# Kernel optimization log

Hardware: AMD Instinct MI355X
Metric: run time of the kernel (lower is better)

## Reference

```python
import jax, jax.numpy as jnp
import numpy as np

N, CT, C, L, H, W, HEAD, GROUPS = 4, 512, 512, 256, 64, 64, 16, 16


def setup_inputs() -> dict:
    key = jax.random.key(0)
    ks = jax.random.split(key, 8)
    d_in_g = C // GROUPS
    return {
        "feature": jax.random.normal(ks[0], (N, C, H, W), dtype=jnp.float32),
        "token": jax.random.normal(ks[1], (N, CT, L), dtype=jnp.float32),
        # conv1x1_1d value/key projections: weight [C_out, C_in]
        "Wv": jax.random.normal(ks[2], (C, CT), dtype=jnp.float32) * (1.0 / np.sqrt(CT)),
        "bv": jnp.zeros((C,), dtype=jnp.float32),
        "Wk": jax.random.normal(ks[3], (C, CT), dtype=jnp.float32) * (1.0 / np.sqrt(CT)),
        "bk": jnp.zeros((C,), dtype=jnp.float32),
        # grouped conv1x1_2d query projection: weight [groups, C_out/g, C_in/g]
        "Wq": jax.random.normal(ks[4], (GROUPS, d_in_g, d_in_g), dtype=jnp.float32) * (1.0 / np.sqrt(d_in_g)),
        "bq": jnp.zeros((C,), dtype=jnp.float32),
    }


def reference(feature, token, Wv, bv, Wk, bk, Wq, bq):
    h = HEAD
    d = C // h              # per-head dim
    S = H * W               # query positions
    # value / key: 1x1 conv1d == matmul over channel dim
    proj_v = (jnp.einsum('oc,ncl->nol', Wv, token) + bv[None, :, None]).reshape(N, h, d, L)
    proj_k = (jnp.einsum('oc,ncl->nol', Wk, token) + bk[None, :, None]).reshape(N, h, d, L)
    # query: grouped 1x1 conv2d (padding=0; see notes) == per-group matmul
    f_g = feature.reshape(N, GROUPS, C // GROUPS, S)
    q = jnp.einsum('goi,ngis->ngos', Wq, f_g).reshape(N, C, S) + bq[None, :, None]
    proj_q = q.reshape(N, h, d, S).transpose(0, 1, 3, 2)  # [N, h, S, d]
    scale = 1.0 / np.sqrt(C / h)
    scores = jnp.einsum('nhsd,nhdl->nhsl', proj_q, proj_k) * scale  # [N,h,S,L]
    proj_coef = jax.nn.softmax(scores, axis=3)
    proj = jnp.einsum('nhdl,nhsl->nhds', proj_v, proj_coef)  # [N,h,d,S]
    return feature + proj.reshape(N, C, H, W)
```

## Files before the change

### kernel.cpp

```cpp
#include <hip/hip_runtime.h>

typedef float f32x4 __attribute__((ext_vector_type(4)));
typedef short bf16x8 __attribute__((ext_vector_type(8)));
typedef __bf16 bf2 __attribute__((ext_vector_type(2)));
typedef unsigned short u16;
typedef unsigned int u32;

#define CT_ 512
#define C_ 512
#define L_ 256
#define S_ 4096
#define D_ 32

static __device__ __forceinline__ u16 f2bf(float x) {
    union { __bf16 h; u16 u; } v; v.h = (__bf16)x; return v.u;
}
static __device__ __forceinline__ u32 packbf(float a, float b) {
    union { bf2 h; u32 u; } v;
    v.h[0] = (__bf16)a; v.h[1] = (__bf16)b;
    return v.u;
}

__global__ __launch_bounds__(256) void prep_all(const float* __restrict__ Wv,
                                                const float* __restrict__ Wk,
                                                const float* __restrict__ token,
                                                u16* __restrict__ wbf,
                                                u16* __restrict__ tokT) {
    __shared__ float tile[32][33];
    int bx = blockIdx.x;
    int t = threadIdx.x;
    if (bx < 256) {
        int idx = (bx * 256 + t) * 8;
        const float* src = (idx < 262144) ? (Wv + idx) : (Wk + (idx - 262144));
        float4 a = *(const float4*)src;
        float4 b = *(const float4*)(src + 4);
        uint4 o;
        o.x = packbf(a.x, a.y);
        o.y = packbf(a.z, a.w);
        o.z = packbf(b.x, b.y);
        o.w = packbf(b.z, b.w);
        *(uint4*)(wbf + idx) = o;
    } else {
        int b2 = bx - 256;
        int ct_t = b2 & 15, l_t = (b2 >> 4) & 7, n = b2 >> 7;
        int r = t >> 3, c4 = (t & 7) * 4;
        const float* src = token + ((size_t)n * CT_ + ct_t * 32 + r) * L_ + l_t * 32 + c4;
        float4 v = *(const float4*)src;
        tile[r][c4] = v.x; tile[r][c4 + 1] = v.y; tile[r][c4 + 2] = v.z; tile[r][c4 + 3] = v.w;
        __syncthreads();
        uint2 o;
        o.x = packbf(tile[c4][r],     tile[c4 + 1][r]);
        o.y = packbf(tile[c4 + 2][r], tile[c4 + 3][r]);
        *(uint2*)(tokT + ((size_t)n * L_ + l_t * 32 + r) * CT_ + ct_t * 32 + c4) = o;
    }
}

__global__ __launch_bounds__(64) void kv_gemm(const u16* __restrict__ Wv_bf,
                                              const u16* __restrict__ Wk_bf,
                                              const u16* __restrict__ tokT,
                                              const float* __restrict__ bv,
                                              const float* __restrict__ bk,
                                              u16* __restrict__ V_hs,
                                              u16* __restrict__ KT_hs) {
    int bx = blockIdx.x;
    int xcd = bx & 7, slot = bx >> 3;
    int l_t = slot & 7, hb = (slot >> 3) & 1, kv = (slot >> 4) & 1, n = slot >> 5;
    int c_t = (hb << 3) | xcd;
    const u16* W = kv ? Wk_bf : Wv_bf;
    const float* bias = kv ? bk : bv;
    int c0 = c_t * 32, l0 = l_t * 32;
    int lane = threadIdx.x;
    int lr = lane & 15, g = lane >> 4;

    const f32x4 fz = {0.f, 0.f, 0.f, 0.f};
    f32x4 acc[2][2] = {{fz, fz}, {fz, fz}};

    const u16* Abase = W + (size_t)(c0 + lr) * CT_ + g * 8;
    const u16* Bbase = tokT + ((size_t)n * L_ + l0 + lr) * CT_ + g * 8;

#pragma unroll
    for (int k = 0; k < 16; ++k) {
        bf16x8 a0 = *(const bf16x8*)(Abase + k * 32);
        bf16x8 a1 = *(const bf16x8*)(Abase + (size_t)16 * CT_ + k * 32);
        bf16x8 b0 = *(const bf16x8*)(Bbase + k * 32);
        bf16x8 b1 = *(const bf16x8*)(Bbase + (size_t)16 * CT_ + k * 32);
        acc[0][0] = __builtin_amdgcn_mfma_f32_16x16x32_bf16(a0, b0, acc[0][0], 0, 0, 0);
        acc[0][1] = __builtin_amdgcn_mfma_f32_16x16x32_bf16(a0, b1, acc[0][1], 0, 0, 0);
        acc[1][0] = __builtin_amdgcn_mfma_f32_16x16x32_bf16(a1, b0, acc[1][0], 0, 0, 0);
        acc[1][1] = __builtin_amdgcn_mfma_f32_16x16x32_bf16(a1, b1, acc[1][1], 0, 0, 0);
    }

    float bb[2][4];
#pragma unroll
    for (int ci = 0; ci < 2; ++ci)
#pragma unroll
        for (int r = 0; r < 4; ++r) bb[ci][r] = bias[c0 + ci * 16 + g * 4 + r];

    if (kv == 0) {
#pragma unroll
        for (int ci = 0; ci < 2; ++ci)
#pragma unroll
            for (int jt = 0; jt < 2; ++jt) {
                int o = jt * 16 + lr;
                int c = o >> 2, q = o & 3;
                int ip = ((c >> 2) & 1) | ((c & 3) << 1);
                int dst_l = l0 + ip * 4 + q;
#pragma unroll
                for (int r = 0; r < 4; ++r) {
                    int d = ci * 16 + g * 4 + r;
                    V_hs[(((size_t)n * 16 + c_t) * D_ + d) * L_ + dst_l] =
                        f2bf(acc[ci][jt][r] + bb[ci][r]);
                }
            }
    } else {
#pragma unroll
        for (int jt = 0; jt < 2; ++jt) {
            int l = l0 + jt * 16 + lr;
#pragma unroll
            for (int ci = 0; ci < 2; ++ci) {
                uint2 o;
                o.x = packbf(acc[ci][jt][0] + bb[ci][0], acc[ci][jt][1] + bb[ci][1]);
                o.y = packbf(acc[ci][jt][2] + bb[ci][2], acc[ci][jt][3] + bb[ci][3]);
                *(uint2*)(KT_hs + (((size_t)n * 16 + c_t) * L_ + l) * D_
                          + g * 8 + ci * 4) = o;
            }
        }
    }
}

__global__ __launch_bounds__(256, 4) void attn(const float* __restrict__ feature,
                                               const float* __restrict__ Wq,
                                               const float* __restrict__ bq,
                                               const u16* __restrict__ V_hs,
                                               const u16* __restrict__ KT_hs,
                                               float* __restrict__ out) {
    __shared__ u16 KT_lds[256][40];
    __shared__ u16 V_lds[32][296];

    int bx = blockIdx.x;
    int xcd = bx & 7, slot = bx >> 3;
    int sb = slot & 31, hb = (slot >> 5) & 1, n = slot >> 6;
    int h = (hb << 3) | xcd;
    int s_base = sb * 128;
    int t = threadIdx.x;
    int w = t >> 6, lane = t & 63, lr = lane & 15, g = lane >> 4;
    const f32x4 fz = {0.f, 0.f, 0.f, 0.f};

    {
        const u16* kbase = KT_hs + ((size_t)n * 16 + h) * (L_ * D_);
#pragma unroll
        for (int i = 0; i < 4; ++i) {
            uint4 v = *(const uint4*)(kbase + ((size_t)i * 256 + t) * 8);
            *(uint4*)&KT_lds[i * 64 + (t >> 2)][(t & 3) * 8] = v;
        }
    }
    {
        const u16* vbase = V_hs + ((size_t)n * 16 + h) * (D_ * L_);
#pragma unroll
        for (int i = 0; i < 4; ++i) {
            uint4 v = *(const uint4*)(vbase + ((size_t)i * 256 + t) * 8);
            *(uint4*)&V_lds[i * 8 + (t >> 5)][(t & 31) * 8] = v;
        }
    }

    const float scale = 0.17677669529663687f * 1.4426950408889634f;
    union { u32 d[4]; bf16x8 v; } wqf[2];
#pragma unroll
    for (int dt = 0; dt < 2; ++dt) {
        const float* wsrc = Wq + ((size_t)h * D_ + dt * 16 + lr) * D_ + g * 8;
        float4 w0 = *(const float4*)wsrc;
        float4 w1 = *(const float4*)(wsrc + 4);
        wqf[dt].d[0] = packbf(w0.x * scale, w0.y * scale);
        wqf[dt].d[1] = packbf(w0.z * scale, w0.w * scale);
        wqf[dt].d[2] = packbf(w1.x * scale, w1.y * scale);
        wqf[dt].d[3] = packbf(w1.z * scale, w1.w * scale);
    }
    f32x4 bqc[2];
#pragma unroll
    for (int dt = 0; dt < 2; ++dt)
#pragma unroll
        for (int r = 0; r < 4; ++r)
            bqc[dt][r] = bq[h * D_ + dt * 16 + g * 4 + r] * scale;

    const float* fb = feature + ((size_t)n * C_ + h * D_) * S_ + s_base + w * 16 + lr;
    float f0[8], f1[8];
#pragma unroll
    for (int j = 0; j < 8; ++j) f0[j] = fb[(size_t)(g * 8 + j) * S_];
#pragma unroll
    for (int j = 0; j < 8; ++j) f1[j] = fb[(size_t)(g * 8 + j) * S_ + 64];

    __syncthreads();

#pragma unroll
    for (int tile = 0; tile < 2; ++tile) {
        int s0 = s_base + tile * 64;

        union { u32 d[4]; bf16x8 v; } au;
#pragma unroll
        for (int k = 0; k < 4; ++k)
            au.d[k] = tile == 0 ? packbf(f0[2 * k], f0[2 * k + 1])
                                : packbf(f1[2 * k], f1[2 * k + 1]);

        f32x4 aq0 = __builtin_amdgcn_mfma_f32_16x16x32_bf16(wqf[0].v, au.v, bqc[0], 0, 0, 0);
        f32x4 aq1 = __builtin_amdgcn_mfma_f32_16x16x32_bf16(wqf[1].v, au.v, bqc[1], 0, 0, 0);
        union { u32 d[4]; bf16x8 v; } qb;
        qb.d[0] = packbf(aq0[0], aq0[1]);
        qb.d[1] = packbf(aq0[2], aq0[3]);
        qb.d[2] = packbf(aq1[0], aq1[1]);
        qb.d[3] = packbf(aq1[2], aq1[3]);

        size_t eoff0 = ((size_t)n * C_ + h * D_ + lr) * S_ + s0 + w * 16 + g * 4;
        size_t eoff1 = eoff0 + (size_t)16 * S_;
        float4 fe0 = *(const float4*)(feature + eoff0);
        float4 fe1 = *(const float4*)(feature + eoff1);

        f32x4 accs[16];
#pragma unroll
        for (int lt = 0; lt < 16; ++lt) {
            bf16x8 a = *(const bf16x8*)&KT_lds[lt * 16 + lr][g * 8];
            accs[lt] = __builtin_amdgcn_mfma_f32_16x16x32_bf16(a, qb.v, fz, 0, 0, 0);
        }

        float s4[4] = {0.f, 0.f, 0.f, 0.f};
#pragma unroll
        for (int lt = 0; lt < 16; ++lt) {
#pragma unroll
            for (int r = 0; r < 4; ++r) {
                float e = __builtin_amdgcn_exp2f(accs[lt][r]);
                accs[lt][r] = e;
                s4[r] += e;
            }
        }
        float sum = (s4[0] + s4[1]) + (s4[2] + s4[3]);
        sum += __shfl_xor(sum, 16, 64);
        sum += __shfl_xor(sum, 32, 64);
        float inv_own = __builtin_amdgcn_rcpf(sum);

        f32x4 acc4[2][2] = {{fz, fz}, {fz, fz}};
#pragma unroll
        for (int tc = 0; tc < 8; ++tc) {
            union { u32 d[4]; bf16x8 v; } pa;
#pragma unroll
            for (int j = 0; j < 4; ++j)
                pa.d[j] = packbf(accs[2 * tc + (j >> 1)][(j & 1) * 2],
                                 accs[2 * tc + (j >> 1)][(j & 1) * 2 + 1]);
#pragma unroll
            for (int dt = 0; dt < 2; ++dt) {
                bf16x8 vb = *(const bf16x8*)&V_lds[dt * 16 + lr][tc * 32 + g * 8];
                acc4[dt][tc & 1] =
                    __builtin_amdgcn_mfma_f32_16x16x32_bf16(pa.v, vb, acc4[dt][tc & 1], 0, 0, 0);
            }
        }
        f32x4 acco[2];
        acco[0] = acc4[0][0] + acc4[0][1];
        acco[1] = acc4[1][0] + acc4[1][1];

        float inv4[4];
#pragma unroll
        for (int r = 0; r < 4; ++r)
            inv4[r] = __shfl(inv_own, (lane & 48) | (g * 4 + r), 64);
        float4 o0, o1;
        o0.x = fe0.x + acco[0][0] * inv4[0];
        o0.y = fe0.y + acco[0][1] * inv4[1];
        o0.z = fe0.z + acco[0][2] * inv4[2];
        o0.w = fe0.w + acco[0][3] * inv4[3];
        o1.x = fe1.x + acco[1][0] * inv4[0];
        o1.y = fe1.y + acco[1][1] * inv4[1];
        o1.z = fe1.z + acco[1][2] * inv4[2];
        o1.w = fe1.w + acco[1][3] * inv4[3];
        *(float4*)(out + eoff0) = o0;
        *(float4*)(out + eoff1) = o1;

        if (tile == 0) __syncthreads();
    }
}

extern "C" void kernel_launch(void* const* d_in, const int* in_sizes, int n_in,
                              void* d_out, int out_size, void* d_ws, size_t ws_size,
                              hipStream_t stream) {
    const float* feature = (const float*)d_in[0];
    const float* token   = (const float*)d_in[1];
    const float* Wv      = (const float*)d_in[2];
    const float* bv      = (const float*)d_in[3];
    const float* Wk      = (const float*)d_in[4];
    const float* bk      = (const float*)d_in[5];
    const float* Wq      = (const float*)d_in[6];
    const float* bq      = (const float*)d_in[7];
    float* out = (float*)d_out;

    u16* ws16  = (u16*)d_ws;
    u16* Wv_bf = ws16;
    u16* Wk_bf = Wv_bf + 262144;
    u16* tokT  = Wk_bf + 262144;
    u16* V_hs  = tokT + 524288;
    u16* KT_hs = V_hs + 524288;

    prep_all<<<dim3(768), dim3(256), 0, stream>>>(Wv, Wk, token, Wv_bf, tokT);
    kv_gemm<<<dim3(1024), dim3(64), 0, stream>>>(Wv_bf, Wk_bf, tokT, bv, bk, V_hs, KT_hs);
    attn<<<dim3(2048), dim3(256), 0, stream>>>(feature, Wq, bq, V_hs, KT_hs, out);
}
```

Baseline: 43.87 us.

## Drop LDS staging in attention; read K/V from global and double grid

```diff
diff --git a/kernel.cpp b/kernel.cpp
--- a/kernel.cpp
+++ b/kernel.cpp
@@ -63,9 +63,7 @@
                                               u16* __restrict__ V_hs,
                                               u16* __restrict__ KT_hs) {
     int bx = blockIdx.x;
-    int xcd = bx & 7, slot = bx >> 3;
-    int l_t = slot & 7, hb = (slot >> 3) & 1, kv = (slot >> 4) & 1, n = slot >> 5;
-    int c_t = (hb << 3) | xcd;
+    int l_t = bx & 7, c_t = (bx >> 3) & 15, kv = (bx >> 7) & 1, n = bx >> 8;
     const u16* W = kv ? Wk_bf : Wv_bf;
     const float* bias = kv ? bk : bv;
     int c0 = c_t * 32, l0 = l_t * 32;
@@ -134,34 +132,12 @@
                                                const u16* __restrict__ V_hs,
                                                const u16* __restrict__ KT_hs,
                                                float* __restrict__ out) {
-    __shared__ u16 KT_lds[256][40];
-    __shared__ u16 V_lds[32][296];
-
     int bx = blockIdx.x;
-    int xcd = bx & 7, slot = bx >> 3;
-    int sb = slot & 31, hb = (slot >> 5) & 1, n = slot >> 6;
-    int h = (hb << 3) | xcd;
-    int s_base = sb * 128;
+    int sb = bx & 63, h = (bx >> 6) & 15, n = bx >> 10;
     int t = threadIdx.x;
     int w = t >> 6, lane = t & 63, lr = lane & 15, g = lane >> 4;
+    int s0 = sb * 64 + w * 16;
     const f32x4 fz = {0.f, 0.f, 0.f, 0.f};
-
-    {
-        const u16* kbase = KT_hs + ((size_t)n * 16 + h) * (L_ * D_);
-#pragma unroll
-        for (int i = 0; i < 4; ++i) {
-            uint4 v = *(const uint4*)(kbase + ((size_t)i * 256 + t) * 8);
-            *(uint4*)&KT_lds[i * 64 + (t >> 2)][(t & 3) * 8] = v;
-        }
-    }
-    {
-        const u16* vbase = V_hs + ((size_t)n * 16 + h) * (D_ * L_);
-#pragma unroll
-        for (int i = 0; i < 4; ++i) {
-            uint4 v = *(const uint4*)(vbase + ((size_t)i * 256 + t) * 8);
-            *(uint4*)&V_lds[i * 8 + (t >> 5)][(t & 31) * 8] = v;
-        }
-    }
 
     const float scale = 0.17677669529663687f * 1.4426950408889634f;
     union { u32 d[4]; bf16x8 v; } wqf[2];
@@ -182,97 +158,92 @@
         for (int r = 0; r < 4; ++r)
             bqc[dt][r] = bq[h * D_ + dt * 16 + g * 4 + r] * scale;
 
-    const float* fb = feature + ((size_t)n * C_ + h * D_) * S_ + s_base + w * 16 + lr;
-    float f0[8], f1[8];
-#pragma unroll
-    for (int j = 0; j < 8; ++j) f0[j] = fb[(size_t)(g * 8 + j) * S_];
-#pragma unroll
-    for (int j = 0; j < 8; ++j) f1[j] = fb[(size_t)(g * 8 + j) * S_ + 64];
-
-    __syncthreads();
-
-#pragma unroll
-    for (int tile = 0; tile < 2; ++tile) {
-        int s0 = s_base + tile * 64;
-
-        union { u32 d[4]; bf16x8 v; } au;
-#pragma unroll
-        for (int k = 0; k < 4; ++k)
-            au.d[k] = tile == 0 ? packbf(f0[2 * k], f0[2 * k + 1])
-                                : packbf(f1[2 * k], f1[2 * k + 1]);
-
-        f32x4 aq0 = __builtin_amdgcn_mfma_f32_16x16x32_bf16(wqf[0].v, au.v, bqc[0], 0, 0, 0);
-        f32x4 aq1 = __builtin_amdgcn_mfma_f32_16x16x32_bf16(wqf[1].v, au.v, bqc[1], 0, 0, 0);
-        union { u32 d[4]; bf16x8 v; } qb;
-        qb.d[0] = packbf(aq0[0], aq0[1]);
-        qb.d[1] = packbf(aq0[2], aq0[3]);
-        qb.d[2] = packbf(aq1[0], aq1[1]);
-        qb.d[3] = packbf(aq1[2], aq1[3]);
-
-        size_t eoff0 = ((size_t)n * C_ + h * D_ + lr) * S_ + s0 + w * 16 + g * 4;
-        size_t eoff1 = eoff0 + (size_t)16 * S_;
-        float4 fe0 = *(const float4*)(feature + eoff0);
-        float4 fe1 = *(const float4*)(feature + eoff1);
-
-        f32x4 accs[16];
-#pragma unroll
-        for (int lt = 0; lt < 16; ++lt) {
-            bf16x8 a = *(const bf16x8*)&KT_lds[lt * 16 + lr][g * 8];
-            accs[lt] = __builtin_amdgcn_mfma_f32_16x16x32_bf16(a, qb.v, fz, 0, 0, 0);
+    const float* fb = feature + ((size_t)n * C_ + h * D_) * S_ + s0 + lr;
+    float f[8];
+#pragma unroll
+    for (int j = 0; j < 8; ++j) f[j] = fb[(size_t)(g * 8 + j) * S_];
+
+    union { u32 d[4]; bf16x8 v; } au;
+#pragma unroll
+    for (int k = 0; k < 4; ++k) au.d[k] = packbf(f[2 * k], f[2 * k + 1]);
+
+    f32x4 aq0 = __builtin_amdgcn_mfma_f32_16x16x32_bf16(wqf[0].v, au.v, bqc[0], 0, 0, 0);
+    f32x4 aq1 = __builtin_amdgcn_mfma_f32_16x16x32_bf16(wqf[1].v, au.v, bqc[1], 0, 0, 0);
+    union { u32 d[4]; bf16x8 v; } qb;
+    qb.d[0] = packbf(aq0[0], aq0[1]);
+    qb.d[1] = packbf(aq0[2], aq0[3]);
+    qb.d[2] = packbf(aq1[0], aq1[1]);
+    qb.d[3] = packbf(aq1[2], aq1[3]);
+
+    size_t eoff0 = ((size_t)n * C_ + h * D_ + lr) * S_ + s0 + g * 4;
+    size_t eoff1 = eoff0 + (size_t)16 * S_;
+    float4 fe0 = *(const float4*)(feature + eoff0);
+    float4 fe1 = *(const float4*)(feature + eoff1);
+
+    const u16* kbase = KT_hs + ((size_t)n * 16 + h) * (L_ * D_) + lr * D_ + g * 8;
+    u32 pa[8][4];
+    float s4[4] = {0.f, 0.f, 0.f, 0.f};
+#pragma unroll
+    for (int tc = 0; tc < 8; ++tc) {
+        bf16x8 k0 = *(const bf16x8*)(kbase + (2 * tc) * (16 * D_));
+        bf16x8 k1 = *(const bf16x8*)(kbase + (2 * tc + 1) * (16 * D_));
+        f32x4 a0 = __builtin_amdgcn_mfma_f32_16x16x32_bf16(k0, qb.v, fz, 0, 0, 0);
+        f32x4 a1 = __builtin_amdgcn_mfma_f32_16x16x32_bf16(k1, qb.v, fz, 0, 0, 0);
+        float e00 = __builtin_amdgcn_exp2f(a0[0]);
+        float e01 = __builtin_amdgcn_exp2f(a0[1]);
+        float e02 = __builtin_amdgcn_exp2f(a0[2]);
+        float e03 = __builtin_amdgcn_exp2f(a0[3]);
+        float e10 = __builtin_amdgcn_exp2f(a1[0]);
+        float e11 = __builtin_amdgcn_exp2f(a1[1]);
+        float e12 = __builtin_amdgcn_exp2f(a1[2]);
+        float e13 = __builtin_amdgcn_exp2f(a1[3]);
+        s4[0] += e00 + e10;
+        s4[1] += e01 + e11;
+        s4[2] += e02 + e12;
+        s4[3] += e03 + e13;
+        pa[tc][0] = packbf(e00, e01);
+        pa[tc][1] = packbf(e02, e03);
+        pa[tc][2] = packbf(e10, e11);
+        pa[tc][3] = packbf(e12, e13);
+    }
+    float sum = (s4[0] + s4[1]) + (s4[2] + s4[3]);
+    sum += __shfl_xor(sum, 16, 64);
+    sum += __shfl_xor(sum, 32, 64);
+    float inv_own = __builtin_amdgcn_rcpf(sum);
+
+    const u16* vbase = V_hs + ((size_t)n * 16 + h) * (D_ * L_) + lr * L_ + g * 8;
+    f32x4 acc4[2][2] = {{fz, fz}, {fz, fz}};
+#pragma unroll
+    for (int tc = 0; tc < 8; ++tc) {
+        union { u32 d[4]; bf16x8 v; } pv;
+        pv.d[0] = pa[tc][0]; pv.d[1] = pa[tc][1];
+        pv.d[2] = pa[tc][2]; pv.d[3] = pa[tc][3];
+#pragma unroll
+        for (int dt = 0; dt < 2; ++dt) {
+            bf16x8 vb = *(const bf16x8*)(vbase + (size_t)dt * (16 * L_) + tc * 32);
+            acc4[dt][tc & 1] =
+                __builtin_amdgcn_mfma_f32_16x16x32_bf16(pv.v, vb, acc4[dt][tc & 1], 0, 0, 0);
         }
-
-        float s4[4] = {0.f, 0.f, 0.f, 0.f};
-#pragma unroll
-        for (int lt = 0; lt < 16; ++lt) {
-#pragma unroll
-            for (int r = 0; r < 4; ++r) {
-                float e = __builtin_amdgcn_exp2f(accs[lt][r]);
-                accs[lt][r] = e;
-                s4[r] += e;
-            }
-        }
-        float sum = (s4[0] + s4[1]) + (s4[2] + s4[3]);
-        sum += __shfl_xor(sum, 16, 64);
-        sum += __shfl_xor(sum, 32, 64);
-        float inv_own = __builtin_amdgcn_rcpf(sum);
-
-        f32x4 acc4[2][2] = {{fz, fz}, {fz, fz}};
-#pragma unroll
-        for (int tc = 0; tc < 8; ++tc) {
-            union { u32 d[4]; bf16x8 v; } pa;
-#pragma unroll
-            for (int j = 0; j < 4; ++j)
-                pa.d[j] = packbf(accs[2 * tc + (j >> 1)][(j & 1) * 2],
-                                 accs[2 * tc + (j >> 1)][(j & 1) * 2 + 1]);
-#pragma unroll
-            for (int dt = 0; dt < 2; ++dt) {
-                bf16x8 vb = *(const bf16x8*)&V_lds[dt * 16 + lr][tc * 32 + g * 8];
-                acc4[dt][tc & 1] =
-                    __builtin_amdgcn_mfma_f32_16x16x32_bf16(pa.v, vb, acc4[dt][tc & 1], 0, 0, 0);
-            }
-        }
-        f32x4 acco[2];
-        acco[0] = acc4[0][0] + acc4[0][1];
-        acco[1] = acc4[1][0] + acc4[1][1];
-
-        float inv4[4];
-#pragma unroll
-        for (int r = 0; r < 4; ++r)
-            inv4[r] = __shfl(inv_own, (lane & 48) | (g * 4 + r), 64);
-        float4 o0, o1;
-        o0.x = fe0.x + acco[0][0] * inv4[0];
-        o0.y = fe0.y + acco[0][1] * inv4[1];
-        o0.z = fe0.z + acco[0][2] * inv4[2];
-        o0.w = fe0.w + acco[0][3] * inv4[3];
-        o1.x = fe1.x + acco[1][0] * inv4[0];
-        o1.y = fe1.y + acco[1][1] * inv4[1];
-        o1.z = fe1.z + acco[1][2] * inv4[2];
-        o1.w = fe1.w + acco[1][3] * inv4[3];
-        *(float4*)(out + eoff0) = o0;
-        *(float4*)(out + eoff1) = o1;
-
-        if (tile == 0) __syncthreads();
-    }
+    }
+    f32x4 acco[2];
+    acco[0] = acc4[0][0] + acc4[0][1];
+    acco[1] = acc4[1][0] + acc4[1][1];
+
+    float inv4[4];
+#pragma unroll
+    for (int r = 0; r < 4; ++r)
+        inv4[r] = __shfl(inv_own, (lane & 48) | (g * 4 + r), 64);
+    float4 o0, o1;
+    o0.x = fe0.x + acco[0][0] * inv4[0];
+    o0.y = fe0.y + acco[0][1] * inv4[1];
+    o0.z = fe0.z + acco[0][2] * inv4[2];
+    o0.w = fe0.w + acco[0][3] * inv4[3];
+    o1.x = fe1.x + acco[1][0] * inv4[0];
+    o1.y = fe1.y + acco[1][1] * inv4[1];
+    o1.z = fe1.z + acco[1][2] * inv4[2];
+    o1.w = fe1.w + acco[1][3] * inv4[3];
+    *(float4*)(out + eoff0) = o0;
+    *(float4*)(out + eoff1) = o1;
 }
 
 extern "C" void kernel_launch(void* const* d_in, const int* in_sizes, int n_in,
@@ -297,5 +268,5 @@
 
     prep_all<<<dim3(768), dim3(256), 0, stream>>>(Wv, Wk, token, Wv_bf, tokT);
     kv_gemm<<<dim3(1024), dim3(64), 0, stream>>>(Wv_bf, Wk_bf, tokT, bv, bk, V_hs, KT_hs);
-    attn<<<dim3(2048), dim3(256), 0, stream>>>(feature, Wq, bq, V_hs, KT_hs, out);
-}
+    attn<<<dim3(4096), dim3(256), 0, stream>>>(feature, Wq, bq, V_hs, KT_hs, out);
+}
```

New measurement: 78.26 us. 1.78x slower.
